# Kernel tuning notes

Hardware: AMD Instinct MI355X
Metric: run time of the kernel (lower is better)

## Reference

```python
import jax, jax.numpy as jnp
import numpy as np

IMG = 640
SCORE_THR = 0.1
IOU_THR = 0.5
MAX_DET = 200  # fixed upper bound on kept boxes per class (jit-static)
BBOX_STD = (0.1, 0.1, 0.2, 0.2)  # standard RetinaNet delta std


def _make_anchors():
    # Standard RetinaNet anchors: P3-P7, 3 ratios x 3 scales, xyxy format.
    strides = [8, 16, 32, 64, 128]
    sizes = [32, 64, 128, 256, 512]
    ratios = np.array([0.5, 1.0, 2.0])
    scales = np.array([2 ** 0, 2 ** (1.0 / 3.0), 2 ** (2.0 / 3.0)])
    out = []
    for stride, size in zip(strides, sizes):
        n = IMG // stride
        ws = (size * scales[None, :] * np.sqrt(1.0 / ratios)[:, None]).reshape(-1)
        hs = (size * scales[None, :] * np.sqrt(ratios)[:, None]).reshape(-1)
        c = (np.arange(n) + 0.5) * stride
        CX, CY = np.meshgrid(c, c)
        ctr = np.stack([CX.ravel(), CY.ravel()], -1)  # [n*n, 2]
        wh = np.stack([ws, hs], -1)  # [9, 2]
        boxes = np.concatenate([ctr[:, None, :] - 0.5 * wh[None],
                                ctr[:, None, :] + 0.5 * wh[None]], -1)  # [n*n, 9, 4]
        out.append(boxes.reshape(-1, 4))
    return np.concatenate(out, 0).astype(np.float32)  # [76725, 4]


def setup_inputs() -> dict:
    key = jax.random.key(0)
    k1, k2 = jax.random.split(key)
    A = 76725
    C = 80
    classification = jax.random.uniform(k1, (1, A, C), dtype=jnp.float32)
    regression = jax.random.normal(k2, (1, A, 4), dtype=jnp.float32)
    anchors = jnp.asarray(_make_anchors())  # [A, 4] xyxy
    return {"classification": classification, "regression": regression, "anchors": anchors}


def _decode_and_clip(anchors, reg):
    aw = anchors[:, 2] - anchors[:, 0]
    ah = anchors[:, 3] - anchors[:, 1]
    ax = anchors[:, 0] + 0.5 * aw
    ay = anchors[:, 1] + 0.5 * ah
    cx = ax + reg[:, 0] * BBOX_STD[0] * aw
    cy = ay + reg[:, 1] * BBOX_STD[1] * ah
    w = aw * jnp.exp(reg[:, 2] * BBOX_STD[2])
    h = ah * jnp.exp(reg[:, 3] * BBOX_STD[3])
    x1 = jnp.clip(cx - 0.5 * w, 0.0, IMG)  # trimBox2Image
    y1 = jnp.clip(cy - 0.5 * h, 0.0, IMG)
    x2 = jnp.clip(cx + 0.5 * w, 0.0, IMG)
    y2 = jnp.clip(cy + 0.5 * h, 0.0, IMG)
    return jnp.stack([x1, y1, x2, y2], -1)  # [A, 4]


def reference(classification, regression, anchors):
    cls = classification[0]  # [A, C]
    boxes = _decode_and_clip(anchors, regression[0])  # [A, 4]
    A = cls.shape[0]
    C = cls.shape[1]
    idx = jnp.arange(A)
    areas = (boxes[:, 2] - boxes[:, 0]) * (boxes[:, 3] - boxes[:, 1])

    def nms_one(scores):  # scores: [A] for one class
        s0 = jnp.where(scores > SCORE_THR, scores, -1.0)
        keep0 = jnp.zeros((A,), dtype=bool)

        def step(carry, _):
            s, keep = carry
            i = jnp.argmax(s)
            valid = s[i] > 0.0
            keep = keep.at[i].set(valid)
            b = boxes[i]
            ix1 = jnp.maximum(b[0], boxes[:, 0])
            iy1 = jnp.maximum(b[1], boxes[:, 1])
            ix2 = jnp.minimum(b[2], boxes[:, 2])
            iy2 = jnp.minimum(b[3], boxes[:, 3])
            inter = jnp.clip(ix2 - ix1, 0.0) * jnp.clip(iy2 - iy1, 0.0)
            ab = (b[2] - b[0]) * (b[3] - b[1])
            iou = inter / (ab + areas - inter)
            sup = valid & ((iou > IOU_THR) | (idx == i))
            s = jnp.where(sup, -1.0, s)
            return (s, keep), None

        (_, keep), _ = jax.lax.scan(step, (s0, keep0), None, length=MAX_DET)
        return keep

    keep = jax.vmap(nms_one)(cls.T)  # [C, A] bool, greedy NMS per class
    final_scores = jnp.where(keep, cls.T, 0.0)  # [C, A]
    final_labels = jnp.where(keep, jnp.arange(C, dtype=jnp.int32)[:, None], -1)  # [C, A]
    final_boxes = jnp.where(keep[..., None], boxes[None], 0.0)  # [C, A, 4]
    return final_scores, final_labels, final_boxes, keep
```

## Files before the change

### kernel.cpp

```cpp
#include <hip/hip_runtime.h>
#include <cstdint>
#include <cstddef>

#pragma clang fp contract(off)

#define A_N 76725
#define C_N 80
#define CA_N (A_N * C_N)
#define MAXDET 200
#define CAP 4096
#define IMG_F 640.0f
#define THR0 0.975f
#define CNT_STRIDE 32

__device__ __forceinline__ bool iou_gt(float b0, float b1, float b2, float b3, float ab,
                                       float x0, float x1, float x2, float x3, float xa) {
    float ix1 = fmaxf(b0, x0);
    float iy1 = fmaxf(b1, x1);
    float ix2 = fminf(b2, x2);
    float iy2 = fminf(b3, x3);
    float iw = fmaxf(ix2 - ix1, 0.0f);
    float ih = fmaxf(iy2 - iy1, 0.0f);
    float inter = iw * ih;
    float den = ab + xa - inter;
    float iou = inter / den;
    return iou > 0.5f;
}

__device__ __forceinline__ float band_lo(int b) {
    return 0.975f - 0.025f * (float)b;
}

__global__ __launch_bounds__(256) void k_prep(const float* __restrict__ cls,
                                              const float* __restrict__ reg,
                                              const float* __restrict__ anc,
                                              float* __restrict__ boxes,
                                              int* __restrict__ gcnt,
                                              unsigned long long* __restrict__ gkeys) {
    int i = blockIdx.x * 256 + threadIdx.x;
    if (i < A_N) {
        float a0 = anc[i * 4 + 0], a1 = anc[i * 4 + 1];
        float a2 = anc[i * 4 + 2], a3 = anc[i * 4 + 3];
        float aw = a2 - a0;
        float ah = a3 - a1;
        float ax = a0 + 0.5f * aw;
        float ay = a1 + 0.5f * ah;
        float r0 = reg[i * 4 + 0], r1 = reg[i * 4 + 1];
        float r2 = reg[i * 4 + 2], r3 = reg[i * 4 + 3];
        float cx = ax + r0 * 0.1f * aw;
        float cy = ay + r1 * 0.1f * ah;
        float w = aw * expf(r2 * 0.2f);
        float h = ah * expf(r3 * 0.2f);
        float x1 = fminf(fmaxf(cx - 0.5f * w, 0.0f), IMG_F);
        float y1 = fminf(fmaxf(cy - 0.5f * h, 0.0f), IMG_F);
        float x2 = fminf(fmaxf(cx + 0.5f * w, 0.0f), IMG_F);
        float y2 = fminf(fmaxf(cy + 0.5f * h, 0.0f), IMG_F);
        boxes[i * 4 + 0] = x1;
        boxes[i * 4 + 1] = y1;
        boxes[i * 4 + 2] = x2;
        boxes[i * 4 + 3] = y2;
    }
    if (i < CA_N) {
        float s = cls[i];
        if (s > THR0) {
            int c = i % C_N;
            unsigned a = (unsigned)(i / C_N);
            int p = atomicAdd(&gcnt[c * CNT_STRIDE], 1);
            if (p < CAP)
                gkeys[(size_t)c * CAP + p] =
                    ((unsigned long long)__float_as_uint(s) << 32) |
                    (unsigned long long)(0xFFFFFFFFu - a);
        }
    }
}

__global__ __launch_bounds__(256) void k_fill(float4* __restrict__ out4) {
    int i = blockIdx.x * 256 + threadIdx.x;
    const int n4 = (7 * CA_N) / 4;
    if (i >= n4) return;
    const int lab_lo = CA_N / 4;
    const int lab_hi = (2 * CA_N) / 4;
    float v = (i >= lab_lo && i < lab_hi) ? -1.0f : 0.0f;
    out4[i] = make_float4(v, v, v, v);
}

__global__ __launch_bounds__(1024) void k_nms(const float* __restrict__ cls,
                                              const float* __restrict__ boxes,
                                              const int* __restrict__ gcnt,
                                              const unsigned long long* __restrict__ gkeys,
                                              float* __restrict__ out) {
    const int c = blockIdx.x;
    const int tid = threadIdx.x;

    __shared__ unsigned long long keys[CAP];
    __shared__ float kbox[MAXDET][4];
    __shared__ float karea[MAXDET];
    __shared__ int kIdxL[MAXDET];
    __shared__ float kScrL[MAXDET];
    __shared__ float cbx[64][4];
    __shared__ float car[64];
    __shared__ unsigned int mlo[64], mhi[64];
    __shared__ unsigned char supp[64];
    __shared__ int cntL, keptL;

    int kept = 0;

    for (int band = 0;; ++band) {
        int cnt;
        bool last = false;
        if (band == 0) {
            cnt = gcnt[c * CNT_STRIDE];
            if (cnt > CAP) cnt = CAP;
            for (int i = tid; i < cnt; i += 1024)
                keys[i] = gkeys[(size_t)c * CAP + i];
            __syncthreads();
        } else {
            float hiB = band_lo(band - 1);
            float lo = band_lo(band);
            last = (lo <= 0.1f);
            float loEff = last ? 0.1f : lo;
            if (tid == 0) cntL = 0;
            __syncthreads();
            for (int a = tid; a < A_N; a += 1024) {
                float s = cls[(size_t)a * C_N + c];
                if (s > loEff && s <= hiB) {
                    int p = atomicAdd(&cntL, 1);
                    if (p < CAP)
                        keys[p] = ((unsigned long long)__float_as_uint(s) << 32) |
                                  (unsigned long long)(0xFFFFFFFFu - (unsigned)a);
                }
            }
            __syncthreads();
            cnt = cntL < CAP ? cntL : CAP;
        }

        int n2 = 64;
        while (n2 < cnt) n2 <<= 1;
        for (int i = cnt + tid; i < n2; i += 1024) keys[i] = 0ull;
        __syncthreads();
        for (int k = 2; k <= n2; k <<= 1) {
            for (int j = k >> 1; j > 0; j >>= 1) {
                for (int i = tid; i < n2; i += 1024) {
                    int ixj = i ^ j;
                    if (ixj > i) {
                        unsigned long long u = keys[i], v = keys[ixj];
                        bool up = ((i & k) == 0);
                        if (up ? (u < v) : (u > v)) { keys[i] = v; keys[ixj] = u; }
                    }
                }
                __syncthreads();
            }
        }

        for (int cs = 0; cs < cnt && kept < MAXDET; cs += 64) {
            int nc = (cnt - cs < 64) ? (cnt - cs) : 64;
            float rb0 = 0, rb1 = 0, rb2 = 0, rb3 = 0, rar = 0, rsc = 0;
            int rix = 0;
            if (tid < 64) {
                mlo[tid] = 0;
                mhi[tid] = 0;
                supp[tid] = (tid < nc) ? 0 : 1;
                if (tid < nc) {
                    unsigned long long key = keys[cs + tid];
                    rix = (int)(0xFFFFFFFFu - (unsigned)(key & 0xFFFFFFFFull));
                    rsc = __uint_as_float((unsigned)(key >> 32));
                    rb0 = boxes[rix * 4 + 0];
                    rb1 = boxes[rix * 4 + 1];
                    rb2 = boxes[rix * 4 + 2];
                    rb3 = boxes[rix * 4 + 3];
                    rar = (rb2 - rb0) * (rb3 - rb1);
                    cbx[tid][0] = rb0; cbx[tid][1] = rb1;
                    cbx[tid][2] = rb2; cbx[tid][3] = rb3;
                    car[tid] = rar;
                }
            }
            __syncthreads();

            {
                int i = tid >> 4, jl = tid & 15;
                if (i < nc) {
                    float x0 = cbx[i][0], x1 = cbx[i][1];
                    float x2 = cbx[i][2], x3 = cbx[i][3], xa = car[i];
                    bool s = false;
                    for (int j = jl; j < kept; j += 16) {
                        if (iou_gt(kbox[j][0], kbox[j][1], kbox[j][2], kbox[j][3],
                                   karea[j], x0, x1, x2, x3, xa)) { s = true; break; }
                    }
                    if (s) supp[i] = 1;
                }
            }
            {
                int i = tid & 63, jb = tid >> 6;
                if (i < nc) {
                    float b0 = cbx[i][0], b1 = cbx[i][1];
                    float b2 = cbx[i][2], b3 = cbx[i][3], ba = car[i];
                    unsigned int l32 = 0, h32 = 0;
                    for (int j = jb; j < nc; j += 16) {
                        if (j > i) {
                            if (iou_gt(b0, b1, b2, b3, ba,
                                       cbx[j][0], cbx[j][1], cbx[j][2], cbx[j][3], car[j])) {
                                if (j < 32) l32 |= 1u << j;
                                else        h32 |= 1u << (j - 32);
                            }
                        }
                    }
                    if (l32) atomicOr(&mlo[i], l32);
                    if (h32) atomicOr(&mhi[i], h32);
                }
            }
            __syncthreads();

            if (tid < 64) {
                int lane = tid;
                bool alive = (lane < nc) && (supp[lane] == 0);
                unsigned int myLo = mlo[lane], myHi = mhi[lane];
                int kc = kept;
                while (kc < MAXDET) {
                    unsigned long long av = __ballot(alive);
                    if (av == 0ull) break;
                    int i = (int)__builtin_ctzll(av);
                    unsigned int plo = (unsigned)__shfl((int)myLo, i, 64);
                    unsigned int phi = (unsigned)__shfl((int)myHi, i, 64);
                    unsigned long long mi = ((unsigned long long)phi << 32) | plo;
                    if (lane == i) {
                        kbox[kc][0] = rb0; kbox[kc][1] = rb1;
                        kbox[kc][2] = rb2; kbox[kc][3] = rb3;
                        karea[kc] = rar;
                        kIdxL[kc] = rix;
                        kScrL[kc] = rsc;
                        alive = false;
                    }
                    if ((mi >> lane) & 1ull) alive = false;
                    kc++;
                }
                if (lane == 0) keptL = kc;
            }
            __syncthreads();
            kept = keptL;
        }

        if (kept >= MAXDET || last) break;
    }

    for (int i = tid; i < kept; i += 1024) {
        int a = kIdxL[i];
        size_t base = (size_t)c * A_N + (size_t)a;
        out[base] = kScrL[i];
        out[(size_t)CA_N + base] = (float)c;
        size_t bo = (size_t)2 * CA_N + base * 4;
        out[bo + 0] = kbox[i][0];
        out[bo + 1] = kbox[i][1];
        out[bo + 2] = kbox[i][2];
        out[bo + 3] = kbox[i][3];
        out[(size_t)6 * CA_N + base] = 1.0f;
    }
}

extern "C" void kernel_launch(void* const* d_in, const int* in_sizes, int n_in,
                              void* d_out, int out_size, void* d_ws, size_t ws_size,
                              hipStream_t stream) {
    const float* cls = (const float*)d_in[0];
    const float* reg = (const float*)d_in[1];
    const float* anc = (const float*)d_in[2];
    float* out = (float*)d_out;

    int* gcnt = (int*)d_ws;
    float* boxes = (float*)(gcnt + C_N * CNT_STRIDE);
    unsigned long long* gkeys =
        (unsigned long long*)(boxes + 4 * A_N);

    hipMemsetAsync(gcnt, 0, C_N * CNT_STRIDE * sizeof(int), stream);

    k_prep<<<(CA_N + 255) / 256, 256, 0, stream>>>(cls, reg, anc, boxes, gcnt, gkeys);

    const int n4 = (7 * CA_N) / 4;
    k_fill<<<(n4 + 255) / 256, 256, 0, stream>>>((float4*)d_out);

    k_nms<<<C_N, 1024, 0, stream>>>(cls, boxes, gcnt, gkeys, out);
}
```

Before: 280.3 us.

## Overlap output fill with per-class NMS and sort small strides within waves

```diff
diff --git a/kernel.cpp b/kernel.cpp
--- a/kernel.cpp
+++ b/kernel.cpp
@@ -12,6 +12,7 @@
 #define IMG_F 640.0f
 #define THR0 0.975f
 #define CNT_STRIDE 32
+#define FILLB 2480
 
 __device__ __forceinline__ bool iou_gt(float b0, float b1, float b2, float b3, float ab,
                                        float x0, float x1, float x2, float x3, float xa) {
@@ -74,23 +75,31 @@
     }
 }
 
-__global__ __launch_bounds__(256) void k_fill(float4* __restrict__ out4) {
-    int i = blockIdx.x * 256 + threadIdx.x;
-    const int n4 = (7 * CA_N) / 4;
-    if (i >= n4) return;
-    const int lab_lo = CA_N / 4;
-    const int lab_hi = (2 * CA_N) / 4;
-    float v = (i >= lab_lo && i < lab_hi) ? -1.0f : 0.0f;
-    out4[i] = make_float4(v, v, v, v);
-}
-
-__global__ __launch_bounds__(1024) void k_nms(const float* __restrict__ cls,
-                                              const float* __restrict__ boxes,
-                                              const int* __restrict__ gcnt,
-                                              const unsigned long long* __restrict__ gkeys,
-                                              float* __restrict__ out) {
+__global__ __launch_bounds__(1024) void k_mega(const float* __restrict__ cls,
+                                               const float* __restrict__ boxes,
+                                               const int* __restrict__ gcnt,
+                                               const unsigned long long* __restrict__ gkeys,
+                                               int* __restrict__ kcnt,
+                                               int* __restrict__ kidx,
+                                               float* __restrict__ kscr,
+                                               float* __restrict__ kboxg,
+                                               float4* __restrict__ out4) {
+    const int tid = threadIdx.x;
+
+    if (blockIdx.x >= C_N) {
+        int fb = blockIdx.x - C_N;
+        const int n4 = (7 * CA_N) / 4;
+        const int lab_lo = CA_N / 4;
+        const int lab_hi = (2 * CA_N) / 4;
+        for (int i = fb * 1024 + tid; i < n4; i += FILLB * 1024) {
+            float v = (i >= lab_lo && i < lab_hi) ? -1.0f : 0.0f;
+            out4[i] = make_float4(v, v, v, v);
+        }
+        return;
+    }
+
     const int c = blockIdx.x;
-    const int tid = threadIdx.x;
+    const int wave = tid >> 6, lane = tid & 63;
 
     __shared__ unsigned long long keys[CAP];
     __shared__ float kbox[MAXDET][4];
@@ -103,6 +112,8 @@
     __shared__ unsigned char supp[64];
     __shared__ int cntL, keptL;
 
+    volatile unsigned long long* vkeys = keys;
+
     int kept = 0;
 
     for (int band = 0;; ++band) {
@@ -134,12 +145,13 @@
             cnt = cntL < CAP ? cntL : CAP;
         }
 
-        int n2 = 64;
+        int n2 = 128;
         while (n2 < cnt) n2 <<= 1;
         for (int i = cnt + tid; i < n2; i += 1024) keys[i] = 0ull;
         __syncthreads();
+
         for (int k = 2; k <= n2; k <<= 1) {
-            for (int j = k >> 1; j > 0; j >>= 1) {
+            for (int j = k >> 1; j >= 64; j >>= 1) {
                 for (int i = tid; i < n2; i += 1024) {
                     int ixj = i ^ j;
                     if (ixj > i) {
@@ -150,6 +162,29 @@
                 }
                 __syncthreads();
             }
+            int segs = n2 >> 7;
+            for (int seg = wave; seg < segs; seg += 16) {
+                int base = seg << 7;
+                int j0 = (k >> 1) < 32 ? (k >> 1) : 32;
+                for (int j = j0; j > 0; j >>= 1) {
+                    int i = base + lane;
+                    int ixj = i ^ j;
+                    if (ixj > i) {
+                        unsigned long long u = vkeys[i], v = vkeys[ixj];
+                        bool up = ((i & k) == 0);
+                        if (up ? (u < v) : (u > v)) { vkeys[i] = v; vkeys[ixj] = u; }
+                    }
+                    i = base + 64 + lane;
+                    ixj = i ^ j;
+                    if (ixj > i) {
+                        unsigned long long u = vkeys[i], v = vkeys[ixj];
+                        bool up = ((i & k) == 0);
+                        if (up ? (u < v) : (u > v)) { vkeys[i] = v; vkeys[ixj] = u; }
+                    }
+                    __builtin_amdgcn_wave_barrier();
+                }
+            }
+            __syncthreads();
         }
 
         for (int cs = 0; cs < cnt && kept < MAXDET; cs += 64) {
@@ -211,7 +246,6 @@
             __syncthreads();
 
             if (tid < 64) {
-                int lane = tid;
                 bool alive = (lane < nc) && (supp[lane] == 0);
                 unsigned int myLo = mlo[lane], myHi = mhi[lane];
                 int kc = kept;
@@ -242,16 +276,34 @@
         if (kept >= MAXDET || last) break;
     }
 
+    if (tid == 0) kcnt[c] = kept;
     for (int i = tid; i < kept; i += 1024) {
-        int a = kIdxL[i];
+        kidx[c * MAXDET + i] = kIdxL[i];
+        kscr[c * MAXDET + i] = kScrL[i];
+        kboxg[(c * MAXDET + i) * 4 + 0] = kbox[i][0];
+        kboxg[(c * MAXDET + i) * 4 + 1] = kbox[i][1];
+        kboxg[(c * MAXDET + i) * 4 + 2] = kbox[i][2];
+        kboxg[(c * MAXDET + i) * 4 + 3] = kbox[i][3];
+    }
+}
+
+__global__ __launch_bounds__(256) void k_scatter(const int* __restrict__ kcnt,
+                                                 const int* __restrict__ kidx,
+                                                 const float* __restrict__ kscr,
+                                                 const float* __restrict__ kboxg,
+                                                 float* __restrict__ out) {
+    int c = blockIdx.x, t = threadIdx.x;
+    int k = kcnt[c];
+    for (int i = t; i < k; i += 256) {
+        int a = kidx[c * MAXDET + i];
         size_t base = (size_t)c * A_N + (size_t)a;
-        out[base] = kScrL[i];
+        out[base] = kscr[c * MAXDET + i];
         out[(size_t)CA_N + base] = (float)c;
         size_t bo = (size_t)2 * CA_N + base * 4;
-        out[bo + 0] = kbox[i][0];
-        out[bo + 1] = kbox[i][1];
-        out[bo + 2] = kbox[i][2];
-        out[bo + 3] = kbox[i][3];
+        out[bo + 0] = kboxg[(c * MAXDET + i) * 4 + 0];
+        out[bo + 1] = kboxg[(c * MAXDET + i) * 4 + 1];
+        out[bo + 2] = kboxg[(c * MAXDET + i) * 4 + 2];
+        out[bo + 3] = kboxg[(c * MAXDET + i) * 4 + 3];
         out[(size_t)6 * CA_N + base] = 1.0f;
     }
 }
@@ -268,13 +320,17 @@
     float* boxes = (float*)(gcnt + C_N * CNT_STRIDE);
     unsigned long long* gkeys =
         (unsigned long long*)(boxes + 4 * A_N);
+    int* kcnt = (int*)(gkeys + (size_t)C_N * CAP);
+    int* kidx = kcnt + C_N;
+    float* kscr = (float*)(kidx + C_N * MAXDET);
+    float* kboxg = kscr + C_N * MAXDET;
 
     hipMemsetAsync(gcnt, 0, C_N * CNT_STRIDE * sizeof(int), stream);
 
     k_prep<<<(CA_N + 255) / 256, 256, 0, stream>>>(cls, reg, anc, boxes, gcnt, gkeys);
 
-    const int n4 = (7 * CA_N) / 4;
-    k_fill<<<(n4 + 255) / 256, 256, 0, stream>>>((float4*)d_out);
-
-    k_nms<<<C_N, 1024, 0, stream>>>(cls, boxes, gcnt, gkeys, out);
-}
+    k_mega<<<C_N + FILLB, 1024, 0, stream>>>(cls, boxes, gcnt, gkeys,
+                                             kcnt, kidx, kscr, kboxg, (float4*)d_out);
+
+    k_scatter<<<C_N, 256, 0, stream>>>(kcnt, kidx, kscr, kboxg, out);
+}
```

New measurement: 287.8 us. 2.7% more time.
